# Performance work log

Hardware: AMD Instinct MI355X
Metric: run time of the kernel (lower is better)

Reference implementation:

```python
import jax, jax.numpy as jnp
import numpy as np

B, L, K = 4096, 4096, 10


def _sparsemax(z):
    # z: [..., n]; Martins & Astudillo sparsemax along last dim
    n = z.shape[-1]
    zs = -jnp.sort(-z, axis=-1)                      # descending
    cum = jnp.cumsum(zs, axis=-1)
    r = jnp.arange(1, n + 1, dtype=z.dtype)
    support = (1.0 + r * zs) > cum                   # [..., n]
    ksel = jnp.sum(support, axis=-1, keepdims=True)  # support size
    tau = (jnp.take_along_axis(cum, ksel - 1, axis=-1) - 1.0) / ksel.astype(z.dtype)
    return jnp.maximum(z - tau, 0.0)


def _topk_bitvectors(logits, k):
    # k highest-scoring binary vectors z in {0,1}^L under <z, logits>
    # (faithful to the CPU batched_topk: detached logits)
    lg = jax.lax.stop_gradient(logits)
    b, latent = lg.shape
    base = (lg > 0).astype(lg.dtype)                 # argmax config [B, L]
    costs = jnp.abs(lg)                              # flip costs
    neg_small, pos = jax.lax.top_k(-costs, k)        # k smallest costs + positions
    c_small = -neg_small                             # [B, k]
    m = 1 << k                                       # 2^k candidate flip subsets
    bits = ((jnp.arange(m)[:, None] >> jnp.arange(k)[None, :]) & 1).astype(lg.dtype)  # [2^k, k]
    sums = jnp.einsum('mk,bk->bm', bits, c_small)    # total flip cost per subset
    _, best = jax.lax.top_k(-sums, k)                # k cheapest subsets [B, k]
    flips = bits[best]                               # [B, k, k] which small-cost bits to flip
    base_at = jnp.take_along_axis(base, pos, axis=1) # base bit value at flip positions [B, k]
    delta = flips * (1.0 - 2.0 * base_at[:, None, :])  # +1 or -1 where flipped
    bv = jnp.broadcast_to(base[:, None, :], (b, k, latent))
    bidx = jnp.arange(b)[:, None, None]
    cidx = jnp.arange(k)[None, :, None]
    jpos = pos[:, None, :]                           # [B, 1, k]
    bv = bv.at[bidx, cidx, jpos].add(delta)          # scatter flips -> [B, k, L]
    return bv


def reference(logits, k):
    bv = _topk_bitvectors(logits, k)                         # [B, k, L]
    scores = jnp.einsum('bkj,bj->bk', bv, logits)            # [B, k]
    distr = _sparsemax(scores)                               # [B, k]
    p = distr.reshape(-1)
    safe_p = jnp.where(p > 0, p, 1.0)
    entropy = -jnp.sum(jnp.where(p > 0, p * jnp.log(safe_p), 0.0))
    batch_size = logits.shape[0]
    return bv, distr, entropy / batch_size


def setup_inputs() -> dict:
    key = jax.random.key(0)
    logits = jax.random.normal(key, (B, L), dtype=jnp.float32)
    return {"logits": logits, "k": K}
```

## Files before the change

kernel.cpp:

```cpp
#include <hip/hip_runtime.h>
#include <stdint.h>

#define NB   4096
#define LDIM 4096
#define KK   10
#define TPB  256

__global__ __launch_bounds__(TPB) void topk_sparsemax(
    const float* __restrict__ logits,
    float* __restrict__ bv,
    float* __restrict__ distr,
    float* __restrict__ ent)
{
    __shared__ unsigned long long s_cand[4 * KK];
    __shared__ float s_wsum[4];
    __shared__ int   s_pos[KK];
    __shared__ int   s_sign[KK];
    __shared__ int   s_bestm[KK];

    const int b    = blockIdx.x;
    const int t    = threadIdx.x;
    const int lane = t & 63;
    const int wv   = t >> 6;
    const float* __restrict__ row = logits + (size_t)b * LDIM;

    float vals[16];
#pragma unroll
    for (int q = 0; q < 4; q++) {
        const float4 f = *(const float4*)(row + (q << 10) + (t << 2));
        vals[q*4+0] = f.x; vals[q*4+1] = f.y; vals[q*4+2] = f.z; vals[q*4+3] = f.w;
    }

    float4 base4[4];
#pragma unroll
    for (int q = 0; q < 4; q++) {
        base4[q].x = vals[q*4+0] > 0.f ? 1.f : 0.f;
        base4[q].y = vals[q*4+1] > 0.f ? 1.f : 0.f;
        base4[q].z = vals[q*4+2] > 0.f ? 1.f : 0.f;
        base4[q].w = vals[q*4+3] > 0.f ? 1.f : 0.f;
    }
    float* out0 = bv + (size_t)b * (KK * LDIM);
#pragma unroll
    for (int c = 0; c < KK; c++) {
        float* orow = out0 + c * LDIM + (t << 2);
#pragma unroll
        for (int q = 0; q < 4; q++)
            *(float4*)(orow + (q << 10)) = base4[q];
    }

    float s0 = 0.f;
#pragma unroll
    for (int i = 0; i < 16; i++) s0 += vals[i] > 0.f ? vals[i] : 0.f;
#pragma unroll
    for (int off = 1; off < 64; off <<= 1) s0 += __shfl_xor(s0, off, 64);
    if (lane == 0) s_wsum[wv] = s0;

    unsigned int taken = 0u;
    for (int c = 0; c < KK; c++) {
        unsigned long long best = ~0ull;
#pragma unroll
        for (int i = 0; i < 16; i++) {
            if (!(taken & (1u << i))) {
                const float val  = vals[i];
                const float cost = fabsf(val);
                const int   idx  = ((i >> 2) << 10) + (t << 2) + (i & 3);
                const unsigned long long pk =
                    ((unsigned long long)__float_as_uint(cost) << 32)
                    | (unsigned)((idx << 1) | (val > 0.f ? 1 : 0));
                if (pk < best) best = pk;
            }
        }
#pragma unroll
        for (int off = 1; off < 64; off <<= 1) {
            const unsigned long long o = __shfl_xor(best, off, 64);
            if (o < best) best = o;
        }
        if (lane == 0) s_cand[wv * KK + c] = best;
        const unsigned lo = (unsigned)best;
        const int idx = (int)(lo >> 1);
        const int rem = idx & 1023;
        if ((rem >> 2) == t) taken |= 1u << (((idx >> 10) << 2) | (rem & 3));
    }
    __syncthreads();

    if (wv == 0) {
        unsigned long long cand = (lane < 4 * KK) ? s_cand[lane] : ~0ull;
        float csm[KK]; int pos[KK]; int sgn[KK];
#pragma unroll
        for (int c = 0; c < KK; c++) {
            unsigned long long w = cand;
#pragma unroll
            for (int off = 1; off < 64; off <<= 1) {
                const unsigned long long o = __shfl_xor(w, off, 64);
                if (o < w) w = o;
            }
            if (cand == w) cand = ~0ull;
            const unsigned lo = (unsigned)w;
            pos[c] = (int)(lo >> 1);
            sgn[c] = (int)(lo & 1u);
            csm[c] = __uint_as_float((unsigned)(w >> 32));
        }

        float sums[16];
#pragma unroll
        for (int i = 0; i < 16; i++) {
            const int m = (lane << 4) | i;
            float acc = 0.f;
#pragma unroll
            for (int j = 0; j < KK; j++) acc += (m & (1 << j)) ? csm[j] : 0.f;
            sums[i] = acc;
        }
        unsigned int taken2 = 0u;
        int bm[KK]; float cst[KK];
        for (int c = 0; c < KK; c++) {
            unsigned long long best = ~0ull;
#pragma unroll
            for (int i = 0; i < 16; i++) {
                if (!(taken2 & (1u << i))) {
                    const unsigned long long pk =
                        ((unsigned long long)__float_as_uint(sums[i]) << 32)
                        | (unsigned)((lane << 4) | i);
                    if (pk < best) best = pk;
                }
            }
#pragma unroll
            for (int off = 1; off < 64; off <<= 1) {
                const unsigned long long o = __shfl_xor(best, off, 64);
                if (o < best) best = o;
            }
            const int m = (int)(unsigned)best;
            if ((m >> 4) == lane) taken2 |= 1u << (m & 15);
            bm[c]  = m;
            cst[c] = __uint_as_float((unsigned)(best >> 32));
        }

        if (lane == 0) {
#pragma unroll
            for (int c = 0; c < KK; c++) {
                s_pos[c] = pos[c]; s_sign[c] = sgn[c]; s_bestm[c] = bm[c];
            }
            const float S0 = (s_wsum[0] + s_wsum[1]) + (s_wsum[2] + s_wsum[3]);
            float z[KK];
#pragma unroll
            for (int c = 0; c < KK; c++) z[c] = S0 - cst[c];
            float acc = 0.f; int ks = 0;
#pragma unroll
            for (int r = 1; r <= KK; r++) {
                acc += z[r-1];
                if (1.f + (float)r * z[r-1] > acc) ks++;
            }
            float acc2 = 0.f;
#pragma unroll
            for (int r = 0; r < KK; r++) if (r < ks) acc2 += z[r];
            const float tau = (acc2 - 1.f) / (float)ks;
            float entl = 0.f;
            float* drow = distr + b * KK;
#pragma unroll
            for (int c = 0; c < KK; c++) {
                float p = z[c] - tau;
                p = p > 0.f ? p : 0.f;
                drow[c] = p;
                if (p > 0.f) entl -= p * logf(p);
            }
            atomicAdd(ent, entl * (1.0f / (float)NB));
        }
    }
    __syncthreads();

    if (t < KK * KK) {
        const int c = t / KK, j = t % KK;
        if ((s_bestm[c] >> j) & 1)
            out0[c * LDIM + s_pos[j]] = s_sign[j] ? 0.f : 1.f;
    }
}

extern "C" void kernel_launch(void* const* d_in, const int* in_sizes, int n_in,
                              void* d_out, int out_size, void* d_ws, size_t ws_size,
                              hipStream_t stream)
{
    const float* logits = (const float*)d_in[0];
    float* out   = (float*)d_out;
    float* bv    = out;
    float* distr = out + (size_t)NB * KK * LDIM;
    float* ent   = distr + (size_t)NB * KK;
    hipMemsetAsync(ent, 0, sizeof(float), stream);
    topk_sparsemax<<<dim3(NB), dim3(TPB), 0, stream>>>(logits, bv, distr, ent);
}
```

Before: 726.9 us.

## Split selection and bitvector writes into separate kernels with deterministic entropy reduction

Splits the fused kernel into three. A selection/sparsemax kernel writes per-row flip metadata and per-row entropy to workspace. A separate bv_write kernel with a (K, B) grid rereads the logits and writes the base bits plus flips for each candidate row. A single-block kernel then reduces entropy in place of the global atomic. This spreads the large bitvector write over many more blocks so it can overlap across rows, at the cost of rereading logits ten times, extra launches, and a workspace round-trip.

Measured after the change: 802.5 us. 1.1x slower.

```diff
diff --git a/kernel.cpp b/kernel.cpp
--- a/kernel.cpp
+++ b/kernel.cpp
@@ -6,17 +6,17 @@
 #define KK   10
 #define TPB  256
 
-__global__ __launch_bounds__(TPB) void topk_sparsemax(
+#define META_STRIDE 32
+#define ENT_OFF     (NB * META_STRIDE)
+
+__global__ __launch_bounds__(TPB) void select_sparsemax(
     const float* __restrict__ logits,
-    float* __restrict__ bv,
-    float* __restrict__ distr,
-    float* __restrict__ ent)
+    int*   __restrict__ meta,
+    float* __restrict__ ent_rows,
+    float* __restrict__ distr)
 {
     __shared__ unsigned long long s_cand[4 * KK];
     __shared__ float s_wsum[4];
-    __shared__ int   s_pos[KK];
-    __shared__ int   s_sign[KK];
-    __shared__ int   s_bestm[KK];
 
     const int b    = blockIdx.x;
     const int t    = threadIdx.x;
@@ -29,23 +29,6 @@
     for (int q = 0; q < 4; q++) {
         const float4 f = *(const float4*)(row + (q << 10) + (t << 2));
         vals[q*4+0] = f.x; vals[q*4+1] = f.y; vals[q*4+2] = f.z; vals[q*4+3] = f.w;
-    }
-
-    float4 base4[4];
-#pragma unroll
-    for (int q = 0; q < 4; q++) {
-        base4[q].x = vals[q*4+0] > 0.f ? 1.f : 0.f;
-        base4[q].y = vals[q*4+1] > 0.f ? 1.f : 0.f;
-        base4[q].z = vals[q*4+2] > 0.f ? 1.f : 0.f;
-        base4[q].w = vals[q*4+3] > 0.f ? 1.f : 0.f;
-    }
-    float* out0 = bv + (size_t)b * (KK * LDIM);
-#pragma unroll
-    for (int c = 0; c < KK; c++) {
-        float* orow = out0 + c * LDIM + (t << 2);
-#pragma unroll
-        for (int q = 0; q < 4; q++)
-            *(float4*)(orow + (q << 10)) = base4[q];
     }
 
     float s0 = 0.f;
@@ -135,9 +118,12 @@
         }
 
         if (lane == 0) {
+            int* mrow = meta + b * META_STRIDE;
 #pragma unroll
             for (int c = 0; c < KK; c++) {
-                s_pos[c] = pos[c]; s_sign[c] = sgn[c]; s_bestm[c] = bm[c];
+                mrow[c]           = pos[c];
+                mrow[KK + c]      = sgn[c];
+                mrow[2 * KK + c]  = bm[c];
             }
             const float S0 = (s_wsum[0] + s_wsum[1]) + (s_wsum[2] + s_wsum[3]);
             float z[KK];
@@ -162,16 +148,60 @@
                 drow[c] = p;
                 if (p > 0.f) entl -= p * logf(p);
             }
-            atomicAdd(ent, entl * (1.0f / (float)NB));
-        }
-    }
+            ent_rows[b] = entl;
+        }
+    }
+}
+
+__global__ __launch_bounds__(TPB) void bv_write(
+    const float* __restrict__ logits,
+    const int*   __restrict__ meta,
+    float*       __restrict__ bv)
+{
+    const int c   = blockIdx.x;
+    const int row = blockIdx.y;
+    const int t   = threadIdx.x;
+    const float* __restrict__ lrow = logits + (size_t)row * LDIM;
+    float* __restrict__ orow = bv + ((size_t)row * KK + c) * LDIM;
+
+#pragma unroll
+    for (int q = 0; q < 4; q++) {
+        const float4 f = *(const float4*)(lrow + (q << 10) + (t << 2));
+        float4 o;
+        o.x = f.x > 0.f ? 1.f : 0.f;
+        o.y = f.y > 0.f ? 1.f : 0.f;
+        o.z = f.z > 0.f ? 1.f : 0.f;
+        o.w = f.w > 0.f ? 1.f : 0.f;
+        *(float4*)(orow + (q << 10) + (t << 2)) = o;
+    }
+
     __syncthreads();
-
-    if (t < KK * KK) {
-        const int c = t / KK, j = t % KK;
-        if ((s_bestm[c] >> j) & 1)
-            out0[c * LDIM + s_pos[j]] = s_sign[j] ? 0.f : 1.f;
-    }
+    if (t < KK) {
+        const int* mrow = meta + row * META_STRIDE;
+        const int bm = mrow[2 * KK + c];
+        if ((bm >> t) & 1) {
+            const int pos = mrow[t];
+            const int sgn = mrow[KK + t];
+            orow[pos] = sgn ? 0.f : 1.f;
+        }
+    }
+}
+
+__global__ __launch_bounds__(TPB) void ent_reduce(
+    const float* __restrict__ ent_rows,
+    float* __restrict__ ent)
+{
+    __shared__ float s_w[4];
+    const int t = threadIdx.x, lane = t & 63, wv = t >> 6;
+    float s = 0.f;
+#pragma unroll
+    for (int i = 0; i < NB / TPB; i++) s += ent_rows[i * TPB + t];
+#pragma unroll
+    for (int off = 1; off < 64; off <<= 1) s += __shfl_xor(s, off, 64);
+    if (lane == 0) s_w[wv] = s;
+    __syncthreads();
+    if (t == 0)
+        ent[0] = ((s_w[0] + s_w[1]) + (s_w[2] + s_w[3])) * (1.0f / (float)NB);
 }
 
 extern "C" void kernel_launch(void* const* d_in, const int* in_sizes, int n_in,
@@ -183,6 +213,10 @@
     float* bv    = out;
     float* distr = out + (size_t)NB * KK * LDIM;
     float* ent   = distr + (size_t)NB * KK;
-    hipMemsetAsync(ent, 0, sizeof(float), stream);
-    topk_sparsemax<<<dim3(NB), dim3(TPB), 0, stream>>>(logits, bv, distr, ent);
-}
+    int*   meta     = (int*)d_ws;
+    float* ent_rows = (float*)d_ws + ENT_OFF;
+
+    select_sparsemax<<<dim3(NB), dim3(TPB), 0, stream>>>(logits, meta, ent_rows, distr);
+    bv_write<<<dim3(KK, NB), dim3(TPB), 0, stream>>>(logits, meta, bv);
+    ent_reduce<<<dim3(1), dim3(TPB), 0, stream>>>(ent_rows, ent);
+}
```
